# Performance work log

Measured on AMD Instinct MI355X. Metric: run time of the kernel, lower is better.

The kernel has to match this reference:

```python
import jax, jax.numpy as jnp
import numpy as np

N_NODES = 50000
N_EDGES = 800000
VOCAB = 32000
IN_FEATS = 128
N_HIDDEN = 128
N_CLASSES = 40
SEQ_LEN = 20
PAD_IX = 0


def setup_inputs() -> dict:
    key = jax.random.key(0)
    ks = jax.random.split(key, 6)
    features = jax.random.randint(ks[0], (N_NODES, SEQ_LEN), 0, VOCAB, dtype=jnp.int64 if jax.config.jax_enable_x64 else jnp.int32).astype(jnp.int32)
    src = jax.random.randint(ks[1], (N_EDGES,), 0, N_NODES, dtype=jnp.int32)
    dst = jax.random.randint(ks[2], (N_EDGES,), 0, N_NODES, dtype=jnp.int32)
    emb_weight = jax.random.normal(ks[3], (VOCAB, IN_FEATS), dtype=jnp.float32) * 0.02
    emb_weight = emb_weight.at[PAD_IX].set(0.0)  # padding_idx row is zero
    W1 = jax.random.normal(ks[4], (IN_FEATS, N_HIDDEN), dtype=jnp.float32) * (1.0 / np.sqrt(IN_FEATS))
    b1 = jnp.zeros((N_HIDDEN,), dtype=jnp.float32)
    W2 = jax.random.normal(ks[5], (N_HIDDEN, N_CLASSES), dtype=jnp.float32) * (1.0 / np.sqrt(N_HIDDEN))
    b2 = jnp.zeros((N_CLASSES,), dtype=jnp.float32)
    return {"features": features, "src": src, "dst": dst, "emb_weight": emb_weight,
            "W1": W1, "b1": b1, "W2": W2, "b2": b2}


def _graph_conv(h, src, dst, W, b, n_nodes, activation=None):
    # DGL GraphConv with norm='both': D_out^{-1/2} applied to src feats,
    # sum-aggregate along edges, D_in^{-1/2} on dst, then linear (+bias, act).
    ones = jnp.ones(src.shape[0], dtype=h.dtype)
    out_deg = jax.ops.segment_sum(ones, src, num_segments=n_nodes)
    in_deg = jax.ops.segment_sum(ones, dst, num_segments=n_nodes)
    h = h * jax.lax.rsqrt(jnp.maximum(out_deg, 1.0))[:, None]
    agg = jax.ops.segment_sum(h[src], dst, num_segments=n_nodes)  # gather + scatter-add (SpMM)
    agg = agg * jax.lax.rsqrt(jnp.maximum(in_deg, 1.0))[:, None]
    out = agg @ W + b
    if activation is not None:
        out = activation(out)
    return out


def reference(features, src, dst, emb_weight, W1, b1, W2, b2):
    n_nodes = features.shape[0]
    # embedding mean-pool over non-pad tokens: [n_nodes, seq, d] -> [n_nodes, d]
    seq_len = jnp.maximum(jnp.sum(features != PAD_IX, axis=1, keepdims=True), 1).astype(emb_weight.dtype)
    h = jnp.take(emb_weight, features, axis=0).sum(axis=1) / seq_len
    h = _graph_conv(h, src, dst, W1, b1, n_nodes, activation=jax.nn.relu)
    # dropout is identity in eval mode
    h = _graph_conv(h, src, dst, W2, b2, n_nodes)
    return h
```

## Files before the change

kernel.cpp:

```cpp
#include <hip/hip_runtime.h>
#include <math.h>

#define N_NODES 50000
#define N_EDGES 800000
#define IN_FEATS 128
#define N_HIDDEN 128
#define N_CLASSES 40
#define SEQ_LEN 20
#define VOCAB 32000
#define BUCKET_CAP 64

#define NPART 196
#define PCAP 4608
#define EGS_BLOCKS 892
#define POOL_BLOCKS 12500
#define POOLCOUNT_BLOCKS (NPART + POOL_BLOCKS)
#define PREP_BLOCKS 89
#define GEMM2_BLOCKS 782

typedef __attribute__((ext_vector_type(8))) short bf16x8;
typedef __attribute__((ext_vector_type(4))) float f32x4;

#define AS1 __attribute__((address_space(1)))
#define AS3 __attribute__((address_space(3)))

__device__ __forceinline__ void gld_lds16(const void* g, void* l) {
    __builtin_amdgcn_global_load_lds((const AS1 unsigned int*)g,
                                     (AS3 unsigned int*)l, 16, 0, 0);
}
__device__ __forceinline__ void vm_wait0() {
    asm volatile("s_waitcnt vmcnt(0)" ::: "memory");
}

__device__ inline unsigned short f2bf(float x) {
    union { float f; unsigned int u; } v; v.f = x;
    unsigned int r = v.u + 0x7FFF + ((v.u >> 16) & 1);
    return (unsigned short)(r >> 16);
}
__device__ inline float bf2f(unsigned short b) {
    union { float f; unsigned int u; } v; v.u = ((unsigned int)b) << 16;
    return v.f;
}


__global__ __launch_bounds__(256) void prep_kernel(
        int4* __restrict__ pcnt_zero, const float* __restrict__ W1,
        unsigned short* __restrict__ W1p, const float* __restrict__ W2,
        unsigned short* __restrict__ W2p) {
    int b = blockIdx.x;
    int t = threadIdx.x;
    if (b == 0) {
        if (t < 128) pcnt_zero[t] = make_int4(0, 0, 0, 0);
    } else if (b < 65) {
        int i = (b - 1) * 256 + t;
        int tile = i >> 9, rem = i & 511;
        int ln = rem >> 3, j = rem & 7;
        int nt = tile >> 2, kb = tile & 3;
        int k = kb * 32 + ((ln >> 4) << 3) + j;
        int n = nt * 16 + (ln & 15);
        W1p[i] = f2bf(W1[k * 128 + n]);
    } else {
        int i = (b - 65) * 256 + t;
        int tile = i >> 9, rem = i & 511;
        int ln = rem >> 3, j = rem & 7;
        int nt = tile >> 2, kb = tile & 3;
        int k = kb * 32 + ((ln >> 4) << 3) + j;
        int n = nt * 16 + (ln & 15);
        W2p[i] = (n < N_CLASSES) ? f2bf(W2[k * N_CLASSES + n]) : (unsigned short)0;
    }
}

__global__ __launch_bounds__(256) void egemm_scat_kernel(
        const int* __restrict__ src, const int* __restrict__ dst,
        unsigned int* __restrict__ pcnt_s, unsigned char* __restrict__ pbuf_s,
        unsigned int* __restrict__ pcnt_d, unsigned int* __restrict__ pbuf_d,
        const float* __restrict__ emb, const unsigned short* __restrict__ W1p,
        unsigned short* __restrict__ Ep) {
    __shared__ unsigned int shm[512];
    int b = blockIdx.x;
    int t = threadIdx.x;
    if (b < 196) {
        unsigned int* lhist = shm;
        unsigned int* lbase = shm + 256;
        for (int i = t; i < NPART; i += 256) lhist[i] = 0u;
        __syncthreads();
        int base = b * 4096;
        int pid[16]; unsigned int rank[16]; unsigned char val[16];
        #pragma unroll
        for (int k = 0; k < 16; ++k) {
            int i = base + k * 256 + t;
            pid[k] = -1;
            if (i < N_EDGES) {
                int u = src[i];
                val[k] = (unsigned char)(u & 255);
                pid[k] = u >> 8;
                rank[k] = atomicAdd(&lhist[pid[k]], 1u);
            }
        }
        __syncthreads();
        for (int i = t; i < NPART; i += 256)
            lbase[i] = atomicAdd(&pcnt_s[i], lhist[i]);
        __syncthreads();
        #pragma unroll
        for (int k = 0; k < 16; ++k) {
            if (pid[k] >= 0) {
                unsigned int pos = lbase[pid[k]] + rank[k];
                if (pos < PCAP) pbuf_s[pid[k] * PCAP + pos] = val[k];
            }
        }
    } else if (b < 392) {
        unsigned int* lhist = shm;
        unsigned int* lbase = shm + 256;
        for (int i = t; i < NPART; i += 256) lhist[i] = 0u;
        __syncthreads();
        int base = (b - 196) * 4096;
        int pid[16]; unsigned int rank[16]; unsigned int val[16];
        #pragma unroll
        for (int k = 0; k < 16; ++k) {
            int i = base + k * 256 + t;
            pid[k] = -1;
            if (i < N_EDGES) {
                int u = src[i];
                int d = dst[i];
                val[k] = ((unsigned int)u << 8) | (unsigned int)(d & 255);
                pid[k] = d >> 8;
                rank[k] = atomicAdd(&lhist[pid[k]], 1u);
            }
        }
        __syncthreads();
        for (int i = t; i < NPART; i += 256)
            lbase[i] = atomicAdd(&pcnt_d[i], lhist[i]);
        __syncthreads();
        #pragma unroll
        for (int k = 0; k < 16; ++k) {
            if (pid[k] >= 0) {
                unsigned int pos = lbase[pid[k]] + rank[k];
                if (pos < PCAP) pbuf_d[pid[k] * PCAP + pos] = val[k];
            }
        }
    } else {
        const int wave = t >> 6, lane = t & 63;
        const int quad = lane >> 4, m = lane & 15;
        const int row0 = (b - 392) * 64 + wave * 16;
        const int arow = row0 + m;
        const float4* ap = (const float4*)(emb + arow * 128 + quad * 8);
        bf16x8 a[4];
        #pragma unroll
        for (int kb = 0; kb < 4; ++kb) {
            float4 x = ap[kb * 8];
            float4 y = ap[kb * 8 + 1];
            bf16x8 tt;
            tt[0] = f2bf(x.x); tt[1] = f2bf(x.y); tt[2] = f2bf(x.z); tt[3] = f2bf(x.w);
            tt[4] = f2bf(y.x); tt[5] = f2bf(y.y); tt[6] = f2bf(y.z); tt[7] = f2bf(y.w);
            a[kb] = tt;
        }
        const int rbase = row0 + quad * 4;
        #pragma unroll
        for (int nt = 0; nt < 8; ++nt) {
            const unsigned short* wp = W1p + (nt * 4) * 512 + lane * 8;
            bf16x8 b0 = *(const bf16x8*)(wp + 0 * 512);
            bf16x8 b1 = *(const bf16x8*)(wp + 1 * 512);
            bf16x8 b2 = *(const bf16x8*)(wp + 2 * 512);
            bf16x8 b3 = *(const bf16x8*)(wp + 3 * 512);
            f32x4 acc = {0.f, 0.f, 0.f, 0.f};
            acc = __builtin_amdgcn_mfma_f32_16x16x32_bf16(a[0], b0, acc, 0, 0, 0);
            acc = __builtin_amdgcn_mfma_f32_16x16x32_bf16(a[1], b1, acc, 0, 0, 0);
            acc = __builtin_amdgcn_mfma_f32_16x16x32_bf16(a[2], b2, acc, 0, 0, 0);
            acc = __builtin_amdgcn_mfma_f32_16x16x32_bf16(a[3], b3, acc, 0, 0, 0);
            #pragma unroll
            for (int r = 0; r < 4; ++r)
                Ep[(rbase + r) * 128 + nt * 16 + m] = f2bf(acc[r]);
        }
    }
}

__global__ __launch_bounds__(256) void poolcount_kernel(
        const unsigned int* __restrict__ pcnt_s, const unsigned char* __restrict__ pbuf_s,
        const unsigned int* __restrict__ pcnt_d, const unsigned int* __restrict__ pbuf_d,
        unsigned int* __restrict__ cnt, float* __restrict__ routf,
        unsigned short* __restrict__ bucketu,
        const int* __restrict__ feats, const unsigned short* __restrict__ Ep,
        unsigned short* __restrict__ G1) {
    __shared__ unsigned int shm[4][SEQ_LEN][64];
    __shared__ int tokl[4][SEQ_LEN];
    int b = blockIdx.x;
    int t = threadIdx.x;
    if (b < NPART) {
        unsigned int* ho = &shm[0][0][0];
        unsigned int* hi_ = &shm[0][0][0] + 256;
        ho[t] = 0u;
        hi_[t] = 0u;
        __syncthreads();
        int p = b;
        int ns = min((int)pcnt_s[p], PCAP);
        const unsigned char* ps = pbuf_s + p * PCAP;
        for (int i = t; i < ns; i += 256) atomicAdd(&ho[ps[i]], 1u);
        int nd = min((int)pcnt_d[p], PCAP);
        const unsigned int* pd = pbuf_d + p * PCAP;
        for (int i = t; i < nd; i += 256) {
            unsigned int e = pd[i];
            unsigned int d = e & 255u;
            unsigned int slot = atomicAdd(&hi_[d], 1u);
            if (slot < BUCKET_CAP)
                bucketu[(p * 256 + (int)d) * BUCKET_CAP + slot] = (unsigned short)(e >> 8);
        }
        __syncthreads();
        int v = p * 256 + t;
        if (v < N_NODES) {
            cnt[v] = (ho[t] << 16) | (hi_[t] & 0xffffu);
            routf[v] = rsqrtf(fmaxf((float)ho[t], 1.f));
        }
        return;
    }
    int w = t >> 6, lane = t & 63;
    int v = (b - NPART) * 4 + w;
    int mytok = 0;
    if (lane < SEQ_LEN) {
        mytok = feats[v * SEQ_LEN + lane];
        tokl[w][lane] = mytok;
    }
    int nz = (int)__popcll(__ballot(lane < SEQ_LEN && mytok != 0));
    __syncthreads();
    #pragma unroll
    for (int g = 0; g < SEQ_LEN / 4; ++g) {
        int tok = tokl[w][4 * g + (lane >> 4)];
        gld_lds16(Ep + tok * 128 + (lane & 15) * 8, &shm[w][4 * g][0]);
    }
    vm_wait0();
    float a0 = 0.f, a1 = 0.f;
    #pragma unroll
    for (int s = 0; s < SEQ_LEN; ++s) {
        unsigned int x = shm[w][s][lane];
        a0 += bf2f((unsigned short)(x & 0xffffu));
        a1 += bf2f((unsigned short)(x >> 16));
    }
    float sc = 1.f / (float)max(nz, 1);
    ushort2 o = {f2bf(a0 * sc), f2bf(a1 * sc)};
    ((ushort2*)G1)[v * 64 + lane] = o;
}

__global__ __launch_bounds__(256) void spmm1_kernel(
        const unsigned int* __restrict__ cnt, const float* __restrict__ routf,
        const unsigned short* __restrict__ bucketu, const unsigned short* __restrict__ G,
        const float* __restrict__ b1, unsigned short* __restrict__ h1) {
    __shared__ unsigned short idxs[256];
    __shared__ unsigned int stg[4][16][64];
    int t = threadIdx.x;
    int node = t >> 6, lane = t & 63;
    int v = blockIdx.x * 4 + node;
    idxs[t] = bucketu[blockIdx.x * 256 + t];
    int ind = (int)(cnt[v] & 0xffffu);
    float rovv = routf[v];
    float2 bb = ((const float2*)b1)[lane];
    int n = min(ind, BUCKET_CAP);
    const unsigned short* bk = &idxs[node * 64];
    float a0 = 0.f, a1 = 0.f;
    for (int base = 0; base < n; base += 16) {
        int m = min(16, n - base);
        int nin = (m + 3) >> 2;
        for (int g = 0; g < nin; ++g) {
            int rc = min(base + 4 * g + (lane >> 4), n - 1);
            int u = bk[rc];
            gld_lds16(G + u * 128 + (lane & 15) * 8, &stg[node][4 * g][0]);
        }
        float rv[16];
        #pragma unroll
        for (int j = 0; j < 16; ++j)
            rv[j] = routf[bk[base + min(j, m - 1)]];
        vm_wait0();
        #pragma unroll
        for (int j = 0; j < 16; ++j) {
            if (j < m) {
                unsigned int x = stg[node][j][lane];
                a0 += bf2f((unsigned short)(x & 0xffffu)) * rv[j];
                a1 += bf2f((unsigned short)(x >> 16)) * rv[j];
            }
        }
    }
    float rin = rsqrtf(fmaxf((float)ind, 1.f));
    float v0 = fmaxf(a0 * rin + bb.x, 0.f) * rovv;
    float v1 = fmaxf(a1 * rin + bb.y, 0.f) * rovv;
    ushort2 o = {f2bf(v0), f2bf(v1)};
    ((ushort2*)h1)[v * 64 + lane] = o;
}

__global__ __launch_bounds__(256) void gemm2_kernel(
        const unsigned short* __restrict__ h1, const unsigned short* __restrict__ W2p,
        unsigned short* __restrict__ G2) {
    const int wave = threadIdx.x >> 6, lane = threadIdx.x & 63;
    const int quad = lane >> 4, m = lane & 15;
    const int row0 = blockIdx.x * 64 + wave * 16;
    const int arow = min(row0 + m, N_NODES - 1);
    const unsigned short* ap = h1 + arow * 128 + quad * 8;
    bf16x8 a0 = *(const bf16x8*)(ap + 0);
    bf16x8 a1 = *(const bf16x8*)(ap + 32);
    bf16x8 a2 = *(const bf16x8*)(ap + 64);
    bf16x8 a3 = *(const bf16x8*)(ap + 96);
    const int rbase = row0 + quad * 4;
    #pragma unroll
    for (int nt = 0; nt < 3; ++nt) {
        const unsigned short* wp = W2p + (nt * 4) * 512 + lane * 8;
        bf16x8 b0 = *(const bf16x8*)(wp + 0 * 512);
        bf16x8 b1 = *(const bf16x8*)(wp + 1 * 512);
        bf16x8 b2 = *(const bf16x8*)(wp + 2 * 512);
        bf16x8 b3 = *(const bf16x8*)(wp + 3 * 512);
        f32x4 acc = {0.f, 0.f, 0.f, 0.f};
        acc = __builtin_amdgcn_mfma_f32_16x16x32_bf16(a0, b0, acc, 0, 0, 0);
        acc = __builtin_amdgcn_mfma_f32_16x16x32_bf16(a1, b1, acc, 0, 0, 0);
        acc = __builtin_amdgcn_mfma_f32_16x16x32_bf16(a2, b2, acc, 0, 0, 0);
        acc = __builtin_amdgcn_mfma_f32_16x16x32_bf16(a3, b3, acc, 0, 0, 0);
        int col = nt * 16 + m;
        #pragma unroll
        for (int r = 0; r < 4; ++r) {
            int row = rbase + r;
            if (row < N_NODES && col < N_CLASSES)
                G2[row * 64 + col] = f2bf(acc[r]);
        }
    }
}

__global__ __launch_bounds__(256) void spmm2_kernel(
        const unsigned int* __restrict__ cnt, const unsigned short* __restrict__ bucketu,
        const unsigned short* __restrict__ G2, const float* __restrict__ b2,
        float* __restrict__ out) {
    __shared__ unsigned short idxs[256];
    __shared__ unsigned short stg[4][32][64];
    int t = threadIdx.x;
    int node = t >> 6, f = t & 63;
    int v = blockIdx.x * 4 + node;
    idxs[t] = bucketu[blockIdx.x * 256 + t];
    int ind = (int)(cnt[v] & 0xffffu);
    int n = min(ind, BUCKET_CAP);
    float acc = 0.f;
    for (int base = 0; base < n; base += 32) {
        int m = min(32, n - base);
        int nin = (m + 7) >> 3;
        for (int g = 0; g < nin; ++g) {
            int rc = min(base + 8 * g + (f >> 3), n - 1);
            int u = idxs[node * 64 + rc];
            gld_lds16(G2 + u * 64 + (f & 7) * 8, &stg[node][8 * g][0]);
        }
        vm_wait0();
        if (f < N_CLASSES) {
            #pragma unroll 4
            for (int j = 0; j < m; ++j) acc += bf2f(stg[node][j][f]);
        }
    }
    if (f < N_CLASSES) {
        float rin = rsqrtf(fmaxf((float)ind, 1.f));
        out[v * N_CLASSES + f] = acc * rin + b2[f];
    }
}

extern "C" void kernel_launch(void* const* d_in, const int* in_sizes, int n_in,
                              void* d_out, int out_size, void* d_ws, size_t ws_size,
                              hipStream_t stream) {
    const int*   feats = (const int*)d_in[0];
    const int*   src   = (const int*)d_in[1];
    const int*   dst   = (const int*)d_in[2];
    const float* emb   = (const float*)d_in[3];
    const float* W1    = (const float*)d_in[4];
    const float* b1    = (const float*)d_in[5];
    const float* W2    = (const float*)d_in[6];
    const float* b2    = (const float*)d_in[7];
    float* out = (float*)d_out;

    char* w = (char*)d_ws;
    unsigned int*   cnt     = (unsigned int*)(w + 0);
    unsigned int*   pcnt_s  = (unsigned int*)(w + 200704);
    unsigned int*   pcnt_d  = (unsigned int*)(w + 201728);
    float*          routf   = (float*)(w + 202752);
    unsigned short* bucketu = (unsigned short*)(w + 403456);
    unsigned char*  pbuf_s  = (unsigned char*)(w + 6803456);
    unsigned int*   pbuf_d  = (unsigned int*)(w + 7706624);
    unsigned short* Ep      = (unsigned short*)(w + 11319296);
    unsigned short* h1      = (unsigned short*)(w + 6803456);
    unsigned short* G1      = (unsigned short*)(w + 19603456);
    unsigned short* G2      = (unsigned short*)(w + 32403456);
    unsigned short* W1p     = (unsigned short*)(w + 38803456);
    unsigned short* W2p     = (unsigned short*)(w + 38836224);

    prep_kernel<<<PREP_BLOCKS, 256, 0, stream>>>((int4*)pcnt_s, W1, W1p, W2, W2p);
    egemm_scat_kernel<<<EGS_BLOCKS, 256, 0, stream>>>(
        src, dst, pcnt_s, pbuf_s, pcnt_d, pbuf_d, emb, W1p, Ep);
    poolcount_kernel<<<POOLCOUNT_BLOCKS, 256, 0, stream>>>(
        pcnt_s, pbuf_s, pcnt_d, pbuf_d, cnt, routf, bucketu, feats, Ep, G1);
    spmm1_kernel<<<POOL_BLOCKS, 256, 0, stream>>>(cnt, routf, bucketu, G1, b1, h1);
    gemm2_kernel<<<GEMM2_BLOCKS, 256, 0, stream>>>(h1, W2p, G2);
    spmm2_kernel<<<POOL_BLOCKS, 256, 0, stream>>>(cnt, bucketu, G2, b2, out);
}
```

Baseline: 185.5 us.

## Fuse layer-2 GEMM into SpMM1, split embedding table halves, compact G2 rows

The layer-2 GEMM now runs inside the SpMM1 kernel. Each block keeps its four aggregated h1 rows in LDS and one wave issues MFMAs against W2, so the h1 round trip through global memory and one launch go away. The projected embedding table is split into two 64-column halves, and pooling runs twice as many blocks, one per half, which shrinks each gather's working set. G2 rows are packed to 40 columns instead of 64, and SpMM2's gather is reshaped to match, cutting gathered bytes at the cost of more complex indexing and an MFMA wave that fills only 4 of its 16 rows.

```diff
diff --git a/kernel.cpp b/kernel.cpp
--- a/kernel.cpp
+++ b/kernel.cpp
@@ -14,9 +14,9 @@
 #define PCAP 4608
 #define EGS_BLOCKS 892
 #define POOL_BLOCKS 12500
-#define POOLCOUNT_BLOCKS (NPART + POOL_BLOCKS)
+#define POOLCOUNT_BLOCKS (NPART + 2 * POOL_BLOCKS)
 #define PREP_BLOCKS 89
-#define GEMM2_BLOCKS 782
+#define SPMM1_BLOCKS 12500
 
 typedef __attribute__((ext_vector_type(8))) short bf16x8;
 typedef __attribute__((ext_vector_type(4))) float f32x4;
@@ -75,7 +75,7 @@
         unsigned int* __restrict__ pcnt_s, unsigned char* __restrict__ pbuf_s,
         unsigned int* __restrict__ pcnt_d, unsigned int* __restrict__ pbuf_d,
         const float* __restrict__ emb, const unsigned short* __restrict__ W1p,
-        unsigned short* __restrict__ Ep) {
+        unsigned short* __restrict__ Ep_lo, unsigned short* __restrict__ Ep_hi) {
     __shared__ unsigned int shm[512];
     int b = blockIdx.x;
     int t = threadIdx.x;
@@ -167,9 +167,11 @@
             acc = __builtin_amdgcn_mfma_f32_16x16x32_bf16(a[1], b1, acc, 0, 0, 0);
             acc = __builtin_amdgcn_mfma_f32_16x16x32_bf16(a[2], b2, acc, 0, 0, 0);
             acc = __builtin_amdgcn_mfma_f32_16x16x32_bf16(a[3], b3, acc, 0, 0, 0);
+            unsigned short* dstp = (nt < 4) ? Ep_lo : Ep_hi;
+            int cofs = (nt & 3) * 16 + m;
             #pragma unroll
             for (int r = 0; r < 4; ++r)
-                Ep[(rbase + r) * 128 + nt * 16 + m] = f2bf(acc[r]);
+                dstp[(rbase + r) * 64 + cofs] = f2bf(acc[r]);
         }
     }
 }
@@ -179,15 +181,15 @@
         const unsigned int* __restrict__ pcnt_d, const unsigned int* __restrict__ pbuf_d,
         unsigned int* __restrict__ cnt, float* __restrict__ routf,
         unsigned short* __restrict__ bucketu,
-        const int* __restrict__ feats, const unsigned short* __restrict__ Ep,
-        unsigned short* __restrict__ G1) {
-    __shared__ unsigned int shm[4][SEQ_LEN][64];
+        const int* __restrict__ feats, const unsigned short* __restrict__ Ep_lo,
+        const unsigned short* __restrict__ Ep_hi, unsigned short* __restrict__ G1) {
+    __shared__ unsigned int ho[256];
+    __shared__ unsigned int hi_[256];
+    __shared__ __align__(16) unsigned short pstg[4][24][64];
     __shared__ int tokl[4][SEQ_LEN];
     int b = blockIdx.x;
     int t = threadIdx.x;
     if (b < NPART) {
-        unsigned int* ho = &shm[0][0][0];
-        unsigned int* hi_ = &shm[0][0][0] + 256;
         ho[t] = 0u;
         hi_[t] = 0u;
         __syncthreads();
@@ -212,8 +214,12 @@
         }
         return;
     }
+    int pq = b - NPART;
+    int half = pq / POOL_BLOCKS;
+    int pb = pq % POOL_BLOCKS;
     int w = t >> 6, lane = t & 63;
-    int v = (b - NPART) * 4 + w;
+    int v = pb * 4 + w;
+    const unsigned short* Eph = half ? Ep_hi : Ep_lo;
     int mytok = 0;
     if (lane < SEQ_LEN) {
         mytok = feats[v * SEQ_LEN + lane];
@@ -222,29 +228,26 @@
     int nz = (int)__popcll(__ballot(lane < SEQ_LEN && mytok != 0));
     __syncthreads();
     #pragma unroll
-    for (int g = 0; g < SEQ_LEN / 4; ++g) {
-        int tok = tokl[w][4 * g + (lane >> 4)];
-        gld_lds16(Ep + tok * 128 + (lane & 15) * 8, &shm[w][4 * g][0]);
+    for (int g = 0; g < 3; ++g) {
+        int rr = min(8 * g + (lane >> 3), SEQ_LEN - 1);
+        int tok = tokl[w][rr];
+        gld_lds16(Eph + tok * 64 + (lane & 7) * 8, &pstg[w][8 * g][0]);
     }
     vm_wait0();
-    float a0 = 0.f, a1 = 0.f;
+    float a = 0.f;
     #pragma unroll
-    for (int s = 0; s < SEQ_LEN; ++s) {
-        unsigned int x = shm[w][s][lane];
-        a0 += bf2f((unsigned short)(x & 0xffffu));
-        a1 += bf2f((unsigned short)(x >> 16));
-    }
-    float sc = 1.f / (float)max(nz, 1);
-    ushort2 o = {f2bf(a0 * sc), f2bf(a1 * sc)};
-    ((ushort2*)G1)[v * 64 + lane] = o;
-}
-
-__global__ __launch_bounds__(256) void spmm1_kernel(
+    for (int s = 0; s < SEQ_LEN; ++s) a += bf2f(pstg[w][s][lane]);
+    G1[v * 128 + half * 64 + lane] = f2bf(a / (float)max(nz, 1));
+}
+
+__global__ __launch_bounds__(256) void spmm1g2_kernel(
         const unsigned int* __restrict__ cnt, const float* __restrict__ routf,
         const unsigned short* __restrict__ bucketu, const unsigned short* __restrict__ G,
-        const float* __restrict__ b1, unsigned short* __restrict__ h1) {
+        const float* __restrict__ b1, const unsigned short* __restrict__ W2p,
+        unsigned short* __restrict__ G2) {
     __shared__ unsigned short idxs[256];
     __shared__ unsigned int stg[4][16][64];
+    __shared__ __align__(16) unsigned short h1b[4][128];
     int t = threadIdx.x;
     int node = t >> 6, lane = t & 63;
     int v = blockIdx.x * 4 + node;
@@ -280,41 +283,33 @@
     float rin = rsqrtf(fmaxf((float)ind, 1.f));
     float v0 = fmaxf(a0 * rin + bb.x, 0.f) * rovv;
     float v1 = fmaxf(a1 * rin + bb.y, 0.f) * rovv;
-    ushort2 o = {f2bf(v0), f2bf(v1)};
-    ((ushort2*)h1)[v * 64 + lane] = o;
-}
-
-__global__ __launch_bounds__(256) void gemm2_kernel(
-        const unsigned short* __restrict__ h1, const unsigned short* __restrict__ W2p,
-        unsigned short* __restrict__ G2) {
-    const int wave = threadIdx.x >> 6, lane = threadIdx.x & 63;
-    const int quad = lane >> 4, m = lane & 15;
-    const int row0 = blockIdx.x * 64 + wave * 16;
-    const int arow = min(row0 + m, N_NODES - 1);
-    const unsigned short* ap = h1 + arow * 128 + quad * 8;
-    bf16x8 a0 = *(const bf16x8*)(ap + 0);
-    bf16x8 a1 = *(const bf16x8*)(ap + 32);
-    bf16x8 a2 = *(const bf16x8*)(ap + 64);
-    bf16x8 a3 = *(const bf16x8*)(ap + 96);
-    const int rbase = row0 + quad * 4;
-    #pragma unroll
-    for (int nt = 0; nt < 3; ++nt) {
-        const unsigned short* wp = W2p + (nt * 4) * 512 + lane * 8;
-        bf16x8 b0 = *(const bf16x8*)(wp + 0 * 512);
-        bf16x8 b1 = *(const bf16x8*)(wp + 1 * 512);
-        bf16x8 b2 = *(const bf16x8*)(wp + 2 * 512);
-        bf16x8 b3 = *(const bf16x8*)(wp + 3 * 512);
-        f32x4 acc = {0.f, 0.f, 0.f, 0.f};
-        acc = __builtin_amdgcn_mfma_f32_16x16x32_bf16(a0, b0, acc, 0, 0, 0);
-        acc = __builtin_amdgcn_mfma_f32_16x16x32_bf16(a1, b1, acc, 0, 0, 0);
-        acc = __builtin_amdgcn_mfma_f32_16x16x32_bf16(a2, b2, acc, 0, 0, 0);
-        acc = __builtin_amdgcn_mfma_f32_16x16x32_bf16(a3, b3, acc, 0, 0, 0);
-        int col = nt * 16 + m;
-        #pragma unroll
-        for (int r = 0; r < 4; ++r) {
-            int row = rbase + r;
-            if (row < N_NODES && col < N_CLASSES)
-                G2[row * 64 + col] = f2bf(acc[r]);
+    h1b[node][2 * lane + 0] = f2bf(v0);
+    h1b[node][2 * lane + 1] = f2bf(v1);
+    __syncthreads();
+    if (t < 64) {
+        const int quad = lane >> 4, m = lane & 15;
+        bf16x8 af[4];
+        #pragma unroll
+        for (int kb = 0; kb < 4; ++kb)
+            af[kb] = *(const bf16x8*)&h1b[m & 3][quad * 8 + kb * 32];
+        #pragma unroll
+        for (int nt = 0; nt < 3; ++nt) {
+            const unsigned short* wp = W2p + (nt * 4) * 512 + lane * 8;
+            bf16x8 b0 = *(const bf16x8*)(wp + 0 * 512);
+            bf16x8 b1f = *(const bf16x8*)(wp + 1 * 512);
+            bf16x8 b2f = *(const bf16x8*)(wp + 2 * 512);
+            bf16x8 b3f = *(const bf16x8*)(wp + 3 * 512);
+            f32x4 acc = {0.f, 0.f, 0.f, 0.f};
+            acc = __builtin_amdgcn_mfma_f32_16x16x32_bf16(af[0], b0, acc, 0, 0, 0);
+            acc = __builtin_amdgcn_mfma_f32_16x16x32_bf16(af[1], b1f, acc, 0, 0, 0);
+            acc = __builtin_amdgcn_mfma_f32_16x16x32_bf16(af[2], b2f, acc, 0, 0, 0);
+            acc = __builtin_amdgcn_mfma_f32_16x16x32_bf16(af[3], b3f, acc, 0, 0, 0);
+            int col = nt * 16 + m;
+            if (quad == 0 && col < N_CLASSES) {
+                #pragma unroll
+                for (int r = 0; r < 4; ++r)
+                    G2[(blockIdx.x * 4 + r) * 40 + col] = f2bf(acc[r]);
+            }
         }
     }
 }
@@ -324,26 +319,32 @@
         const unsigned short* __restrict__ G2, const float* __restrict__ b2,
         float* __restrict__ out) {
     __shared__ unsigned short idxs[256];
-    __shared__ unsigned short stg[4][32][64];
+    __shared__ __align__(16) unsigned short stg[4][3][512];
     int t = threadIdx.x;
     int node = t >> 6, f = t & 63;
     int v = blockIdx.x * 4 + node;
     idxs[t] = bucketu[blockIdx.x * 256 + t];
     int ind = (int)(cnt[v] & 0xffffu);
     int n = min(ind, BUCKET_CAP);
+    int jrow = min(f / 5, 11), jsub = f - jrow * 5;
     float acc = 0.f;
-    for (int base = 0; base < n; base += 32) {
-        int m = min(32, n - base);
-        int nin = (m + 7) >> 3;
-        for (int g = 0; g < nin; ++g) {
-            int rc = min(base + 8 * g + (f >> 3), n - 1);
+    for (int base = 0; base < n; base += 36) {
+        int m = min(36, n - base);
+        int ng = (m + 11) / 12;
+        for (int g = 0; g < ng; ++g) {
+            int rc = min(base + 12 * g + jrow, n - 1);
             int u = idxs[node * 64 + rc];
-            gld_lds16(G2 + u * 64 + (f & 7) * 8, &stg[node][8 * g][0]);
+            gld_lds16(G2 + u * 40 + jsub * 8, &stg[node][g][0]);
         }
         vm_wait0();
         if (f < N_CLASSES) {
-            #pragma unroll 4
-            for (int j = 0; j < m; ++j) acc += bf2f(stg[node][j][f]);
+            for (int g = 0; g < ng; ++g) {
+                #pragma unroll
+                for (int j = 0; j < 12; ++j) {
+                    if (base + 12 * g + j < n)
+                        acc += bf2f(stg[node][g][j * 40 + f]);
+                }
+            }
         }
     }
     if (f < N_CLASSES) {
@@ -373,19 +374,20 @@
     unsigned short* bucketu = (unsigned short*)(w + 403456);
     unsigned char*  pbuf_s  = (unsigned char*)(w + 6803456);
     unsigned int*   pbuf_d  = (unsigned int*)(w + 7706624);
-    unsigned short* Ep      = (unsigned short*)(w + 11319296);
-    unsigned short* h1      = (unsigned short*)(w + 6803456);
-    unsigned short* G1      = (unsigned short*)(w + 19603456);
-    unsigned short* G2      = (unsigned short*)(w + 32403456);
-    unsigned short* W1p     = (unsigned short*)(w + 38803456);
-    unsigned short* W2p     = (unsigned short*)(w + 38836224);
+    unsigned short* Ep_lo   = (unsigned short*)(w + 11319296);
+    unsigned short* Ep_hi   = (unsigned short*)(w + 15415296);
+    unsigned short* G1      = (unsigned short*)(w + 19511296);
+    unsigned short* G2      = (unsigned short*)(w + 32311296);
+    unsigned short* W1p     = (unsigned short*)(w + 36311296);
+    unsigned short* W2p     = (unsigned short*)(w + 36344064);
 
     prep_kernel<<<PREP_BLOCKS, 256, 0, stream>>>((int4*)pcnt_s, W1, W1p, W2, W2p);
     egemm_scat_kernel<<<EGS_BLOCKS, 256, 0, stream>>>(
-        src, dst, pcnt_s, pbuf_s, pcnt_d, pbuf_d, emb, W1p, Ep);
+        src, dst, pcnt_s, pbuf_s, pcnt_d, pbuf_d, emb, W1p, Ep_lo, Ep_hi);
     poolcount_kernel<<<POOLCOUNT_BLOCKS, 256, 0, stream>>>(
-        pcnt_s, pbuf_s, pcnt_d, pbuf_d, cnt, routf, bucketu, feats, Ep, G1);
-    spmm1_kernel<<<POOL_BLOCKS, 256, 0, stream>>>(cnt, routf, bucketu, G1, b1, h1);
-    gemm2_kernel<<<GEMM2_BLOCKS, 256, 0, stream>>>(h1, W2p, G2);
+        pcnt_s, pbuf_s, pcnt_d, pbuf_d, cnt, routf, bucketu,
+        feats, Ep_lo, Ep_hi, G1);
+    spmm1g2_kernel<<<SPMM1_BLOCKS, 256, 0, stream>>>(
+        cnt, routf, bucketu, G1, b1, W2p, G2);
     spmm2_kernel<<<POOL_BLOCKS, 256, 0, stream>>>(cnt, bucketu, G2, b2, out);
 }
```

After: 188.9 us. Within noise of the previous version (+1.9%).
